# Optimization experiments

Hardware: AMD Instinct MI355X
Metric: run time of the kernel (lower is better)

Reference implementation:

```python
import jax, jax.numpy as jnp
import numpy as np

B, S, HID = 1, 2048, 2048
NH = 16
D_NOPE, D_ROPE, D_V = 128, 64, 128
D_QK = D_NOPE + D_ROPE            # 192
KV_R = 512                        # kv_lora_rank
EPS = 1e-6
SCALING = D_QK ** -0.5
NEG = -1e9


def rms_norm(x, w):
    xf = x.astype(jnp.float32)
    var = jnp.mean(xf * xf, axis=-1, keepdims=True)
    return w * (xf * jax.lax.rsqrt(var + EPS)).astype(x.dtype)


def rotate_half(x):
    x1, x2 = jnp.split(x, 2, axis=-1)
    return jnp.concatenate([-x2, x1], axis=-1)


def deinterleave(x):
    # torch: view(..., d//2, 2).transpose(-1, -2).reshape(..., d)
    # => [x0, x2, x4, ..., x1, x3, x5, ...]
    return jnp.concatenate([x[..., 0::2], x[..., 1::2]], axis=-1)


def setup_inputs() -> dict:
    key = jax.random.key(0)
    ks = jax.random.split(key, 6)
    hidden_states = jax.random.normal(ks[0], (B, S, HID), jnp.float32)
    # rotary cos/sin over qk_rope_head_dim
    inv_freq = 1.0 / (10000.0 ** (np.arange(0, D_ROPE, 2, dtype=np.float32) / D_ROPE))
    freqs = np.outer(np.arange(S, dtype=np.float32), inv_freq)   # [S, D_ROPE/2]
    emb = np.concatenate([freqs, freqs], axis=-1)                # [S, D_ROPE]
    cos = jnp.asarray(np.cos(emb), jnp.float32)[None]            # [1, S, D_ROPE]
    sin = jnp.asarray(np.sin(emb), jnp.float32)[None]
    # additive causal mask [1, 1, S, S]
    causal = np.where(np.tril(np.ones((S, S), dtype=bool)), 0.0, NEG).astype(np.float32)
    attention_mask = jnp.asarray(causal)[None, None]
    sc = lambda k, shp: jax.random.normal(k, shp, jnp.float32) * (shp[-1] ** -0.5)
    q_proj_w = sc(ks[1], (NH * D_QK, HID))
    kv_a_proj_w = sc(ks[2], (KV_R + D_ROPE, HID))
    kv_a_ln_w = jnp.ones((KV_R,), jnp.float32)
    kv_b_proj_w = sc(ks[3], (NH * (D_NOPE + D_V), KV_R))
    o_proj_w = sc(ks[4], (HID, NH * D_V))
    return dict(hidden_states=hidden_states, cos=cos, sin=sin,
                attention_mask=attention_mask, q_proj_w=q_proj_w,
                kv_a_proj_w=kv_a_proj_w, kv_a_ln_w=kv_a_ln_w,
                kv_b_proj_w=kv_b_proj_w, o_proj_w=o_proj_w)


def reference(hidden_states, cos, sin, attention_mask,
              q_proj_w, kv_a_proj_w, kv_a_ln_w, kv_b_proj_w, o_proj_w):
    b, s, _ = hidden_states.shape
    # Q projection -> [b, NH, s, D_QK]
    q = (hidden_states @ q_proj_w.T).reshape(b, s, NH, D_QK).transpose(0, 2, 1, 3)
    q_pass, q_rot = q[..., :D_NOPE], q[..., D_NOPE:]
    # compressed KV + shared rope key
    ckv = hidden_states @ kv_a_proj_w.T                           # [b, s, KV_R + D_ROPE]
    k_pass_c, k_rot = ckv[..., :KV_R], ckv[..., KV_R:]
    kv = (rms_norm(k_pass_c, kv_a_ln_w) @ kv_b_proj_w.T)
    kv = kv.reshape(b, s, NH, D_NOPE + D_V).transpose(0, 2, 1, 3)  # [b, NH, s, .]
    k_pass, value_states = kv[..., :D_NOPE], kv[..., D_NOPE:]
    k_rot = k_rot.reshape(b, 1, s, D_ROPE)
    # interleaved RoPE (rope_interleave=True)
    q_rot = deinterleave(q_rot)
    k_rot = deinterleave(k_rot)
    c = cos[:, None]  # [1, 1, s, D_ROPE]
    sn = sin[:, None]
    q_rot = q_rot * c + rotate_half(q_rot) * sn
    k_rot = k_rot * c + rotate_half(k_rot) * sn
    k_rot = jnp.broadcast_to(k_rot, (b, NH, s, D_ROPE))
    query_states = jnp.concatenate([q_pass, q_rot], axis=-1)      # [b, NH, s, D_QK]
    key_states = jnp.concatenate([k_pass, k_rot], axis=-1)
    # eager attention (num_key_value_groups == 1)
    scores = jnp.einsum('bhqd,bhkd->bhqk', query_states, key_states) * SCALING
    scores = scores + attention_mask[:, :, :, :s]
    attn = jax.nn.softmax(scores.astype(jnp.float32), axis=-1).astype(query_states.dtype)
    attn_out = jnp.einsum('bhqk,bhkd->bhqd', attn, value_states)  # [b, NH, s, D_V]
    attn_out = attn_out.transpose(0, 2, 1, 3).reshape(b, s, NH * D_V)
    return attn_out @ o_proj_w.T
```

## Files before the change

### kernel.cpp

```cpp
#include <hip/hip_runtime.h>
#include <hip/hip_bf16.h>
#include <stdint.h>
#include <stddef.h>

#define S_LEN 2048
#define HID_DIM 2048
#define NH 16
#define D_QK 192
#define D_NOPE 128
#define D_ROPE 64
#define D_V 128
#define KV_R 512
#define CKV_N (KV_R + D_ROPE)
#define KVB_N (NH * (D_NOPE + D_V))
#define QN (NH * D_QK)
#define CAT_N (QN + CKV_N)
#define SCALING 0.07216878364870322f

typedef __attribute__((ext_vector_type(8))) short short8;
typedef __attribute__((ext_vector_type(4))) short short4v;
typedef __attribute__((ext_vector_type(4))) float f32x4;

__device__ __forceinline__ short f2bf_bits(float f) {
  unsigned u = __float_as_uint(f);
  unsigned r = (u + 0x7fffu + ((u >> 16) & 1u)) >> 16;
  return (short)(r & 0xffffu);
}
__device__ __forceinline__ float bf2f(short b) {
  return __uint_as_float(((unsigned)(unsigned short)b) << 16);
}

__device__ __forceinline__ f32x4 mfma_bf16(short8 a, short8 b, f32x4 c) {
  return __builtin_amdgcn_mfma_f32_16x16x32_bf16(a, b, c, 0, 0, 0);
}

__global__ __launch_bounds__(256)
void cvt5_k(const float* __restrict__ s0, short* __restrict__ d0, int c0,
            const float* __restrict__ s1, short* __restrict__ d1, int c1,
            const float* __restrict__ s2, short* __restrict__ d2, int c2,
            const float* __restrict__ s3, short* __restrict__ d3, int c3,
            const float* __restrict__ s4, short* __restrict__ d4, int c4) {
  const int i = blockIdx.x * 256 + threadIdx.x;
  const float* s; short* d; int base;
  if      (i < c0) { s = s0; d = d0; base = 0;  }
  else if (i < c1) { s = s1; d = d1; base = c0; }
  else if (i < c2) { s = s2; d = d2; base = c1; }
  else if (i < c3) { s = s3; d = d3; base = c2; }
  else if (i < c4) { s = s4; d = d4; base = c3; }
  else return;
  const int j = i - base;
  const float4 v = ((const float4*)s)[j];
  short4v o;
  o.x = f2bf_bits(v.x); o.y = f2bf_bits(v.y);
  o.z = f2bf_bits(v.z); o.w = f2bf_bits(v.w);
  ((short4v*)d)[j] = o;
}

template <bool OUTF32>
__global__ __launch_bounds__(256, 3)
void gemm_bt(const short* __restrict__ A, const short* __restrict__ B,
             void* __restrict__ Cv, int M, int N, int K) {
  __shared__ short sA[2][128 * 32];
  __shared__ short sB[2][128 * 32];
  const int tid  = threadIdx.x;
  const int wave = tid >> 6;
  const int lane = tid & 63;
  const int bm = blockIdx.y * 128;
  const int bn = blockIdx.x * 128;
  const int wr = wave >> 1, wc = wave & 1;
  const int fr = lane & 15, fk = (lane >> 4) * 8;
  const int srow = lane >> 2;
  const int scol = (lane & 3) * 8;

  f32x4 acc[4][4];
  for (int i = 0; i < 4; ++i)
    for (int j = 0; j < 4; ++j)
      for (int r = 0; r < 4; ++r) acc[i][j][r] = 0.f;

  for (int k0 = 0; k0 < K; k0 += 64) {
    __syncthreads();
#pragma unroll
    for (int cc = 0; cc < 2; ++cc) {
      const int c = wave * 2 + cc;
      const int ar = bm + c * 16 + srow;
      int br = bn + c * 16 + srow; if (br > N - 1) br = N - 1;
#pragma unroll
      for (int kh = 0; kh < 2; ++kh) {
        __builtin_amdgcn_global_load_lds(
            (const __attribute__((address_space(1))) void*)(A + (size_t)ar * K + k0 + kh * 32 + scol),
            (__attribute__((address_space(3))) void*)(sA[kh] + c * 512), 16, 0, 0);
        __builtin_amdgcn_global_load_lds(
            (const __attribute__((address_space(1))) void*)(B + (size_t)br * K + k0 + kh * 32 + scol),
            (__attribute__((address_space(3))) void*)(sB[kh] + c * 512), 16, 0, 0);
      }
    }
    __syncthreads();
#pragma unroll
    for (int kh = 0; kh < 2; ++kh) {
      short8 af[4], bfr[4];
#pragma unroll
      for (int i = 0; i < 4; ++i)
        af[i] = *(const short8*)(sA[kh] + (wr * 64 + i * 16 + fr) * 32 + fk);
#pragma unroll
      for (int j = 0; j < 4; ++j)
        bfr[j] = *(const short8*)(sB[kh] + (wc * 64 + j * 16 + fr) * 32 + fk);
#pragma unroll
      for (int i = 0; i < 4; ++i)
#pragma unroll
        for (int j = 0; j < 4; ++j)
          acc[i][j] = mfma_bf16(af[i], bfr[j], acc[i][j]);
    }
  }

  const int cr = (lane >> 4) * 4, ccol = lane & 15;
#pragma unroll
  for (int i = 0; i < 4; ++i)
#pragma unroll
    for (int j = 0; j < 4; ++j) {
      const int col = bn + wc * 64 + j * 16 + ccol;
      if (col < N) {
#pragma unroll
        for (int r = 0; r < 4; ++r) {
          const int row = bm + wr * 64 + i * 16 + cr + r;
          if (OUTF32)
            ((float*)Cv)[(size_t)row * N + col] = acc[i][j][r];
          else
            ((short*)Cv)[(size_t)row * N + col] = f2bf_bits(acc[i][j][r]);
        }
      }
    }
}

__global__ __launch_bounds__(256)
void rmsnorm_k(const short* __restrict__ qckv, const float* __restrict__ w,
               short* __restrict__ out) {
  const int s = blockIdx.x, t = threadIdx.x;
  const short* x = qckv + (size_t)s * CAT_N + QN;
  float v0 = bf2f(x[2 * t]), v1 = bf2f(x[2 * t + 1]);
  float ss = v0 * v0 + v1 * v1;
#pragma unroll
  for (int off = 1; off < 64; off <<= 1) ss += __shfl_xor(ss, off, 64);
  __shared__ float red[4];
  if ((t & 63) == 0) red[t >> 6] = ss;
  __syncthreads();
  const float tot = red[0] + red[1] + red[2] + red[3];
  const float sc = rsqrtf(tot * (1.0f / 512.0f) + 1e-6f);
  out[(size_t)s * KV_R + 2 * t]     = f2bf_bits(v0 * sc * w[2 * t]);
  out[(size_t)s * KV_R + 2 * t + 1] = f2bf_bits(v1 * sc * w[2 * t + 1]);
}

__global__ __launch_bounds__(256)
void prep_k(const short* __restrict__ qckv, const short* __restrict__ kvb,
            const float* __restrict__ cosb, const float* __restrict__ sinb,
            short* __restrict__ Qs, short* __restrict__ Ks) {
  const int s = blockIdx.x, t = threadIdx.x;
  const short* qrow = qckv + (size_t)s * CAT_N;
  __shared__ float cs[32], sn[32];
  __shared__ short krs[64];
  if (t < 32) {
    const float c  = cosb[(size_t)s * 64 + t];
    const float si = sinb[(size_t)s * 64 + t];
    cs[t] = c; sn[t] = si;
    const float e0 = bf2f(qrow[QN + KV_R + 2 * t]);
    const float e1 = bf2f(qrow[QN + KV_R + 2 * t + 1]);
    krs[t]      = f2bf_bits(e0 * c - e1 * si);
    krs[t + 32] = f2bf_bits(e1 * c + e0 * si);
  }
  __syncthreads();
  const int h = t >> 4, i = t & 15;
  *(short8*)(Qs + ((size_t)h * S_LEN + s) * D_QK + i * 8) =
      *(const short8*)(qrow + h * D_QK + i * 8);
  *(short8*)(Ks + ((size_t)h * S_LEN + s) * D_QK + i * 8) =
      *(const short8*)(kvb + (size_t)s * KVB_N + h * 256 + i * 8);
#pragma unroll
  for (int p = 0; p < 2; ++p) {
    const int ii = i * 2 + p;
    const float e0 = bf2f(qrow[h * D_QK + 128 + 2 * ii]);
    const float e1 = bf2f(qrow[h * D_QK + 128 + 2 * ii + 1]);
    Qs[((size_t)h * S_LEN + s) * D_QK + 128 + ii] = f2bf_bits(e0 * cs[ii] - e1 * sn[ii]);
    Qs[((size_t)h * S_LEN + s) * D_QK + 160 + ii] = f2bf_bits(e1 * cs[ii] + e0 * sn[ii]);
  }
#pragma unroll
  for (int p = 0; p < 4; ++p) {
    const int idx = t * 4 + p;
    const int hh = idx >> 6, ii = idx & 63;
    Ks[((size_t)hh * S_LEN + s) * D_QK + 128 + ii] = krs[ii];
  }
}

__global__ __launch_bounds__(256)
void vtr_k(const short* __restrict__ kvb, short* __restrict__ Vt) {
  const int st = blockIdx.x, dt = blockIdx.y, h = blockIdx.z;
  __shared__ short sT[64][72];
  const int id = threadIdx.x;
#pragma unroll
  for (int p = 0; p < 2; ++p) {
    const int q = id + p * 256;
    const int row = q >> 3, c8 = q & 7;
    *(short8*)(&sT[row][c8 * 8]) =
        *(const short8*)(kvb + (size_t)(st * 64 + row) * KVB_N + h * 256 + 128 + dt * 64 + c8 * 8);
  }
  __syncthreads();
#pragma unroll
  for (int p = 0; p < 2; ++p) {
    const int q = id + p * 256;
    const int drow = q >> 3, c8 = q & 7;
    short8 o;
#pragma unroll
    for (int j = 0; j < 8; ++j) o[j] = sT[c8 * 8 + j][drow];
    *(short8*)(Vt + ((size_t)h * D_V + dt * 64 + drow) * S_LEN + st * 64 + c8 * 8) = o;
  }
}

__global__ __launch_bounds__(256, 1)
void flash_k(const short* __restrict__ Qs, const short* __restrict__ Ks,
             const short* __restrict__ Vt, short* __restrict__ Oc) {
  __shared__ short sK[64 * 200];
  __shared__ short sVt[128 * 72];
  __shared__ short P_lds[4][16 * 72];
  const int tid = threadIdx.x;
  const int wv = tid >> 6;
  const int lane = tid & 63;
  const int blk = blockIdx.x;
  const int h = ((blk & 7) << 1) | ((blk >> 3) & 1);
  const int a = blk >> 4;
  const int b = 31 - a;
  const int fr = lane & 15, g = lane >> 4;
  const int q0[2] = { a * 64 + wv * 16, b * 64 + wv * 16 };

  const short* Qh = Qs + (size_t)h * S_LEN * D_QK;
  const short* Kh = Ks + (size_t)h * S_LEN * D_QK;
  const short* Vh = Vt + (size_t)h * D_V * S_LEN;

  int rowK[6], c8K[6], rowV[4], c8V[4];
#pragma unroll
  for (int p = 0; p < 6; ++p) {
    const int id = tid + p * 256;
    rowK[p] = id / 24; c8K[p] = id % 24;
  }
#pragma unroll
  for (int p = 0; p < 4; ++p) {
    const int id = tid + p * 256;
    rowV[p] = id >> 3; c8V[p] = id & 7;
  }

  short8 qa[2][6];
#pragma unroll
  for (int rt = 0; rt < 2; ++rt)
#pragma unroll
    for (int c = 0; c < 6; ++c)
      qa[rt][c] = *(const short8*)(Qh + (size_t)(q0[rt] + fr) * D_QK + c * 32 + g * 8);

  f32x4 o[2][8];
  float m_i[2][4], l_i[2][4];
#pragma unroll
  for (int rt = 0; rt < 2; ++rt)
#pragma unroll
    for (int r = 0; r < 4; ++r) {
      m_i[rt][r] = -1e30f; l_i[rt][r] = 0.f;
#pragma unroll
      for (int f = 0; f < 8; ++f) o[rt][f][r] = 0.f;
    }

  short8 kc[6], vc[4];
#pragma unroll
  for (int p = 0; p < 6; ++p)
    kc[p] = *(const short8*)(Kh + (size_t)rowK[p] * D_QK + c8K[p] * 8);
#pragma unroll
  for (int p = 0; p < 4; ++p)
    vc[p] = *(const short8*)(Vh + (size_t)rowV[p] * S_LEN + c8V[p] * 8);

  short* pl = &P_lds[wv][0];
  const int jn = b + 1;
  for (int jt = 0; jt < jn; ++jt) {
    const int j0 = jt << 6;
    const bool lightOn = (jt <= a);
    __syncthreads();
#pragma unroll
    for (int p = 0; p < 6; ++p)
      *(short8*)(sK + rowK[p] * 200 + c8K[p] * 8) = kc[p];
#pragma unroll
    for (int p = 0; p < 4; ++p)
      *(short8*)(sVt + rowV[p] * 72 + c8V[p] * 8) = vc[p];
    __syncthreads();
    if (jt + 1 < jn) {
      const int j1 = (jt + 1) << 6;
#pragma unroll
      for (int p = 0; p < 6; ++p)
        kc[p] = *(const short8*)(Kh + (size_t)(j1 + rowK[p]) * D_QK + c8K[p] * 8);
#pragma unroll
      for (int p = 0; p < 4; ++p)
        vc[p] = *(const short8*)(Vh + (size_t)rowV[p] * S_LEN + j1 + c8V[p] * 8);
    }

    f32x4 sc[2][4];
#pragma unroll
    for (int rt = 0; rt < 2; ++rt)
#pragma unroll
      for (int t = 0; t < 4; ++t)
        for (int r = 0; r < 4; ++r) sc[rt][t][r] = -1e30f;
#pragma unroll
    for (int t = 0; t < 4; ++t) {
      const bool hOn = (j0 + t * 16 <= q0[1] + 15);
      const bool lOn = lightOn && (j0 + t * 16 <= q0[0] + 15);
      if (hOn || lOn) {
        short8 kfr[6];
#pragma unroll
        for (int c = 0; c < 6; ++c)
          kfr[c] = *(const short8*)(sK + (t * 16 + fr) * 200 + c * 32 + g * 8);
        if (lOn) {
          f32x4 acc; for (int r = 0; r < 4; ++r) acc[r] = 0.f;
#pragma unroll
          for (int c = 0; c < 6; ++c) acc = mfma_bf16(qa[0][c], kfr[c], acc);
          sc[0][t] = acc;
        }
        if (hOn) {
          f32x4 acc; for (int r = 0; r < 4; ++r) acc[r] = 0.f;
#pragma unroll
          for (int c = 0; c < 6; ++c) acc = mfma_bf16(qa[1][c], kfr[c], acc);
          sc[1][t] = acc;
        }
      }
    }

#pragma unroll
    for (int rt = 0; rt < 2; ++rt) {
      if (rt == 0 && !lightOn) continue;
      const int qq = q0[rt];
      float tm[4];
#pragma unroll
      for (int r = 0; r < 4; ++r) {
        const int row = qq + g * 4 + r;
        float mx = -1e30f;
#pragma unroll
        for (int t = 0; t < 4; ++t) {
          const float v = (j0 + t * 16 + fr <= row) ? sc[rt][t][r] * SCALING : -1e30f;
          sc[rt][t][r] = v;
          mx = fmaxf(mx, v);
        }
        tm[r] = mx;
      }
#pragma unroll
      for (int off = 1; off < 16; off <<= 1)
#pragma unroll
        for (int r = 0; r < 4; ++r)
          tm[r] = fmaxf(tm[r], __shfl_xor(tm[r], off, 16));
      float ps[4];
#pragma unroll
      for (int r = 0; r < 4; ++r) {
        const float mnew = fmaxf(m_i[rt][r], tm[r]);
        const float alpha = __expf(m_i[rt][r] - mnew);
        m_i[rt][r] = mnew;
        l_i[rt][r] *= alpha;
        float s = 0.f;
#pragma unroll
        for (int t = 0; t < 4; ++t) {
          const float p = __expf(sc[rt][t][r] - mnew);
          sc[rt][t][r] = p;
          s += p;
        }
        ps[r] = s;
#pragma unroll
        for (int f = 0; f < 8; ++f) o[rt][f][r] *= alpha;
      }
#pragma unroll
      for (int off = 1; off < 16; off <<= 1)
#pragma unroll
        for (int r = 0; r < 4; ++r)
          ps[r] += __shfl_xor(ps[r], off, 16);
#pragma unroll
      for (int r = 0; r < 4; ++r) l_i[rt][r] += ps[r];

#pragma unroll
      for (int r = 0; r < 4; ++r)
#pragma unroll
        for (int t = 0; t < 4; ++t)
          pl[(g * 4 + r) * 72 + t * 16 + fr] = f2bf_bits(sc[rt][t][r]);
      __builtin_amdgcn_fence(__ATOMIC_ACQ_REL, "wavefront");
      const short8 pa0 = *(const short8*)(pl + fr * 72 + g * 8);
      const short8 pa1 = *(const short8*)(pl + fr * 72 + 32 + g * 8);
#pragma unroll
      for (int f = 0; f < 8; ++f) {
        const short* vr = sVt + (f * 16 + fr) * 72 + g * 8;
        const short8 vb0 = *(const short8*)(vr);
        const short8 vb1 = *(const short8*)(vr + 32);
        o[rt][f] = mfma_bf16(pa1, vb1, mfma_bf16(pa0, vb0, o[rt][f]));
      }
    }
  }

#pragma unroll
  for (int rt = 0; rt < 2; ++rt)
#pragma unroll
    for (int r = 0; r < 4; ++r) {
      const float inv = 1.0f / l_i[rt][r];
      const int row = q0[rt] + g * 4 + r;
#pragma unroll
      for (int f = 0; f < 8; ++f)
        Oc[(size_t)row * (NH * D_V) + h * D_V + f * 16 + fr] = f2bf_bits(o[rt][f][r] * inv);
    }
}

extern "C" void kernel_launch(void* const* d_in, const int* in_sizes, int n_in,
                              void* d_out, int out_size, void* d_ws, size_t ws_size,
                              hipStream_t stream) {
  const float* hidden = (const float*)d_in[0];
  const float* cosb   = (const float*)d_in[1];
  const float* sinb   = (const float*)d_in[2];
  const float* q_w    = (const float*)d_in[4];
  const float* kva_w  = (const float*)d_in[5];
  const float* ln_w   = (const float*)d_in[6];
  const float* kvb_w  = (const float*)d_in[7];
  const float* o_w    = (const float*)d_in[8];
  float* out = (float*)d_out;

  char* ws = (char*)d_ws;
  size_t off = 0;
  auto alloc = [&](size_t elems) {
    short* p = (short*)(ws + off);
    off += ((elems * 2 + 255) & ~(size_t)255);
    return p;
  };
  short* hid_b   = alloc((size_t)S_LEN * HID_DIM);
  short* qkva_wb = alloc((size_t)CAT_N * HID_DIM);
  short* kvb_wb  = alloc((size_t)KVB_N * KV_R);
  short* o_wb    = alloc((size_t)HID_DIM * NH * D_V);
  short* qckv    = alloc((size_t)S_LEN * CAT_N);
  short* ckvn    = alloc((size_t)S_LEN * KV_R);
  short* kvb     = alloc((size_t)S_LEN * KVB_N);
  short* Qs      = alloc((size_t)NH * S_LEN * D_QK);
  short* Ks      = alloc((size_t)NH * S_LEN * D_QK);
  short* Vt      = alloc((size_t)NH * D_V * S_LEN);
  short* Oc      = alloc((size_t)S_LEN * NH * D_V);

  dim3 blk(256);
  const int n0 = (S_LEN * HID_DIM) / 4;
  const int n1 = (QN * HID_DIM) / 4;
  const int n2 = (CKV_N * HID_DIM) / 4;
  const int n3 = (KVB_N * KV_R) / 4;
  const int n4e = (HID_DIM * NH * D_V) / 4;
  const int c0 = n0, c1 = c0 + n1, c2 = c1 + n2, c3 = c2 + n3, c4 = c3 + n4e;
  cvt5_k<<<dim3((c4 + 255) / 256), blk, 0, stream>>>(
      hidden, hid_b, c0,
      q_w, qkva_wb, c1,
      kva_w, qkva_wb + (size_t)QN * HID_DIM, c2,
      kvb_w, kvb_wb, c3,
      o_w, o_wb, c4);

  gemm_bt<false><<<dim3((CAT_N + 127) / 128, S_LEN / 128), blk, 0, stream>>>(
      hid_b, qkva_wb, qckv, S_LEN, CAT_N, HID_DIM);
  rmsnorm_k<<<dim3(S_LEN), blk, 0, stream>>>(qckv, ln_w, ckvn);
  gemm_bt<false><<<dim3(KVB_N / 128, S_LEN / 128), blk, 0, stream>>>(
      ckvn, kvb_wb, kvb, S_LEN, KVB_N, KV_R);
  prep_k<<<dim3(S_LEN), blk, 0, stream>>>(qckv, kvb, cosb, sinb, Qs, Ks);
  vtr_k<<<dim3(S_LEN / 64, D_V / 64, NH), blk, 0, stream>>>(kvb, Vt);
  flash_k<<<dim3(NH * 16), blk, 0, stream>>>(Qs, Ks, Vt, Oc);
  gemm_bt<true><<<dim3(HID_DIM / 128, S_LEN / 128), blk, 0, stream>>>(
      Oc, o_wb, out, S_LEN, HID_DIM, NH * D_V);
}
```

Baseline: 321.1 us.

## Split paired causal query tiles into one tile per block with higher occupancy

The flash attention kernel previously gave each block two 64-row query tiles (a light one and a heavy one paired for causal load balance). Now each block handles a single query tile, the grid grows from 256 to 512 blocks, and launch bounds allow two blocks per CU. This halves per-thread register state so more waves can hide latency and more CUs get work, at the cost of uneven per-block work and each block reloading K/V tiles on its own with no sharing between the two tiles.

```diff
diff --git a/kernel.cpp b/kernel.cpp
--- a/kernel.cpp
+++ b/kernel.cpp
@@ -212,7 +212,7 @@
   }
 }
 
-__global__ __launch_bounds__(256, 1)
+__global__ __launch_bounds__(256, 2)
 void flash_k(const short* __restrict__ Qs, const short* __restrict__ Ks,
              const short* __restrict__ Vt, short* __restrict__ Oc) {
   __shared__ short sK[64 * 200];
@@ -223,10 +223,9 @@
   const int lane = tid & 63;
   const int blk = blockIdx.x;
   const int h = ((blk & 7) << 1) | ((blk >> 3) & 1);
-  const int a = blk >> 4;
-  const int b = 31 - a;
+  const int qb = 31 - (blk >> 4);
+  const int q0 = qb * 64 + wv * 16;
   const int fr = lane & 15, g = lane >> 4;
-  const int q0[2] = { a * 64 + wv * 16, b * 64 + wv * 16 };
 
   const short* Qh = Qs + (size_t)h * S_LEN * D_QK;
   const short* Kh = Ks + (size_t)h * S_LEN * D_QK;
@@ -244,23 +243,16 @@
     rowV[p] = id >> 3; c8V[p] = id & 7;
   }
 
-  short8 qa[2][6];
-#pragma unroll
-  for (int rt = 0; rt < 2; ++rt)
-#pragma unroll
-    for (int c = 0; c < 6; ++c)
-      qa[rt][c] = *(const short8*)(Qh + (size_t)(q0[rt] + fr) * D_QK + c * 32 + g * 8);
-
-  f32x4 o[2][8];
-  float m_i[2][4], l_i[2][4];
-#pragma unroll
-  for (int rt = 0; rt < 2; ++rt)
-#pragma unroll
-    for (int r = 0; r < 4; ++r) {
-      m_i[rt][r] = -1e30f; l_i[rt][r] = 0.f;
-#pragma unroll
-      for (int f = 0; f < 8; ++f) o[rt][f][r] = 0.f;
-    }
+  short8 qa[6];
+#pragma unroll
+  for (int c = 0; c < 6; ++c)
+    qa[c] = *(const short8*)(Qh + (size_t)(q0 + fr) * D_QK + c * 32 + g * 8);
+
+  f32x4 o[8];
+  for (int f = 0; f < 8; ++f)
+    for (int r = 0; r < 4; ++r) o[f][r] = 0.f;
+  float m_i[4] = {-1e30f, -1e30f, -1e30f, -1e30f};
+  float l_i[4] = {0.f, 0.f, 0.f, 0.f};
 
   short8 kc[6], vc[4];
 #pragma unroll
@@ -271,10 +263,9 @@
     vc[p] = *(const short8*)(Vh + (size_t)rowV[p] * S_LEN + c8V[p] * 8);
 
   short* pl = &P_lds[wv][0];
-  const int jn = b + 1;
+  const int jn = qb + 1;
   for (int jt = 0; jt < jn; ++jt) {
     const int j0 = jt << 6;
-    const bool lightOn = (jt <= a);
     __syncthreads();
 #pragma unroll
     for (int p = 0; p < 6; ++p)
@@ -293,112 +284,92 @@
         vc[p] = *(const short8*)(Vh + (size_t)rowV[p] * S_LEN + j1 + c8V[p] * 8);
     }
 
-    f32x4 sc[2][4];
-#pragma unroll
-    for (int rt = 0; rt < 2; ++rt)
+    f32x4 sc[4];
+#pragma unroll
+    for (int t = 0; t < 4; ++t)
+      for (int r = 0; r < 4; ++r) sc[t][r] = -1e30f;
+#pragma unroll
+    for (int t = 0; t < 4; ++t) {
+      if (j0 + t * 16 <= q0 + 15) {
+        f32x4 a;
+        for (int r = 0; r < 4; ++r) a[r] = 0.f;
+        const short* kr = sK + (t * 16 + fr) * 200 + g * 8;
+#pragma unroll
+        for (int c = 0; c < 6; ++c)
+          a = mfma_bf16(qa[c], *(const short8*)(kr + c * 32), a);
+        sc[t] = a;
+      }
+    }
+    float tm[4];
+#pragma unroll
+    for (int r = 0; r < 4; ++r) {
+      const int row = q0 + g * 4 + r;
+      float mx = -1e30f;
+#pragma unroll
+      for (int t = 0; t < 4; ++t) {
+        const float v = (j0 + t * 16 + fr <= row) ? sc[t][r] * SCALING : -1e30f;
+        sc[t][r] = v;
+        mx = fmaxf(mx, v);
+      }
+      tm[r] = mx;
+    }
+#pragma unroll
+    for (int off = 1; off < 16; off <<= 1)
+#pragma unroll
+      for (int r = 0; r < 4; ++r)
+        tm[r] = fmaxf(tm[r], __shfl_xor(tm[r], off, 16));
+    float ps[4];
+#pragma unroll
+    for (int r = 0; r < 4; ++r) {
+      const float mnew = fmaxf(m_i[r], tm[r]);
+      const float alpha = __expf(m_i[r] - mnew);
+      m_i[r] = mnew;
+      l_i[r] *= alpha;
+      float s = 0.f;
+#pragma unroll
+      for (int t = 0; t < 4; ++t) {
+        const float p = __expf(sc[t][r] - mnew);
+        sc[t][r] = p;
+        s += p;
+      }
+      ps[r] = s;
+#pragma unroll
+      for (int f = 0; f < 8; ++f) o[f][r] *= alpha;
+    }
+#pragma unroll
+    for (int off = 1; off < 16; off <<= 1)
+#pragma unroll
+      for (int r = 0; r < 4; ++r)
+        ps[r] += __shfl_xor(ps[r], off, 16);
+#pragma unroll
+    for (int r = 0; r < 4; ++r) l_i[r] += ps[r];
+
+#pragma unroll
+    for (int r = 0; r < 4; ++r)
 #pragma unroll
       for (int t = 0; t < 4; ++t)
-        for (int r = 0; r < 4; ++r) sc[rt][t][r] = -1e30f;
-#pragma unroll
-    for (int t = 0; t < 4; ++t) {
-      const bool hOn = (j0 + t * 16 <= q0[1] + 15);
-      const bool lOn = lightOn && (j0 + t * 16 <= q0[0] + 15);
-      if (hOn || lOn) {
-        short8 kfr[6];
-#pragma unroll
-        for (int c = 0; c < 6; ++c)
-          kfr[c] = *(const short8*)(sK + (t * 16 + fr) * 200 + c * 32 + g * 8);
-        if (lOn) {
-          f32x4 acc; for (int r = 0; r < 4; ++r) acc[r] = 0.f;
-#pragma unroll
-          for (int c = 0; c < 6; ++c) acc = mfma_bf16(qa[0][c], kfr[c], acc);
-          sc[0][t] = acc;
-        }
-        if (hOn) {
-          f32x4 acc; for (int r = 0; r < 4; ++r) acc[r] = 0.f;
-#pragma unroll
-          for (int c = 0; c < 6; ++c) acc = mfma_bf16(qa[1][c], kfr[c], acc);
-          sc[1][t] = acc;
-        }
-      }
-    }
-
-#pragma unroll
-    for (int rt = 0; rt < 2; ++rt) {
-      if (rt == 0 && !lightOn) continue;
-      const int qq = q0[rt];
-      float tm[4];
-#pragma unroll
-      for (int r = 0; r < 4; ++r) {
-        const int row = qq + g * 4 + r;
-        float mx = -1e30f;
-#pragma unroll
-        for (int t = 0; t < 4; ++t) {
-          const float v = (j0 + t * 16 + fr <= row) ? sc[rt][t][r] * SCALING : -1e30f;
-          sc[rt][t][r] = v;
-          mx = fmaxf(mx, v);
-        }
-        tm[r] = mx;
-      }
-#pragma unroll
-      for (int off = 1; off < 16; off <<= 1)
-#pragma unroll
-        for (int r = 0; r < 4; ++r)
-          tm[r] = fmaxf(tm[r], __shfl_xor(tm[r], off, 16));
-      float ps[4];
-#pragma unroll
-      for (int r = 0; r < 4; ++r) {
-        const float mnew = fmaxf(m_i[rt][r], tm[r]);
-        const float alpha = __expf(m_i[rt][r] - mnew);
-        m_i[rt][r] = mnew;
-        l_i[rt][r] *= alpha;
-        float s = 0.f;
-#pragma unroll
-        for (int t = 0; t < 4; ++t) {
-          const float p = __expf(sc[rt][t][r] - mnew);
-          sc[rt][t][r] = p;
-          s += p;
-        }
-        ps[r] = s;
-#pragma unroll
-        for (int f = 0; f < 8; ++f) o[rt][f][r] *= alpha;
-      }
-#pragma unroll
-      for (int off = 1; off < 16; off <<= 1)
-#pragma unroll
-        for (int r = 0; r < 4; ++r)
-          ps[r] += __shfl_xor(ps[r], off, 16);
-#pragma unroll
-      for (int r = 0; r < 4; ++r) l_i[rt][r] += ps[r];
-
-#pragma unroll
-      for (int r = 0; r < 4; ++r)
-#pragma unroll
-        for (int t = 0; t < 4; ++t)
-          pl[(g * 4 + r) * 72 + t * 16 + fr] = f2bf_bits(sc[rt][t][r]);
-      __builtin_amdgcn_fence(__ATOMIC_ACQ_REL, "wavefront");
-      const short8 pa0 = *(const short8*)(pl + fr * 72 + g * 8);
-      const short8 pa1 = *(const short8*)(pl + fr * 72 + 32 + g * 8);
-#pragma unroll
-      for (int f = 0; f < 8; ++f) {
-        const short* vr = sVt + (f * 16 + fr) * 72 + g * 8;
-        const short8 vb0 = *(const short8*)(vr);
-        const short8 vb1 = *(const short8*)(vr + 32);
-        o[rt][f] = mfma_bf16(pa1, vb1, mfma_bf16(pa0, vb0, o[rt][f]));
-      }
-    }
-  }
-
-#pragma unroll
-  for (int rt = 0; rt < 2; ++rt)
-#pragma unroll
-    for (int r = 0; r < 4; ++r) {
-      const float inv = 1.0f / l_i[rt][r];
-      const int row = q0[rt] + g * 4 + r;
-#pragma unroll
-      for (int f = 0; f < 8; ++f)
-        Oc[(size_t)row * (NH * D_V) + h * D_V + f * 16 + fr] = f2bf_bits(o[rt][f][r] * inv);
-    }
+        pl[(g * 4 + r) * 72 + t * 16 + fr] = f2bf_bits(sc[t][r]);
+    __builtin_amdgcn_fence(__ATOMIC_ACQ_REL, "wavefront");
+    const short8 pa0 = *(const short8*)(pl + fr * 72 + g * 8);
+    const short8 pa1 = *(const short8*)(pl + fr * 72 + 32 + g * 8);
+
+#pragma unroll
+    for (int f = 0; f < 8; ++f) {
+      const short* vr = sVt + (f * 16 + fr) * 72 + g * 8;
+      const short8 vb0 = *(const short8*)(vr);
+      const short8 vb1 = *(const short8*)(vr + 32);
+      o[f] = mfma_bf16(pa1, vb1, mfma_bf16(pa0, vb0, o[f]));
+    }
+  }
+
+#pragma unroll
+  for (int r = 0; r < 4; ++r) {
+    const float inv = 1.0f / l_i[r];
+    const int row = q0 + g * 4 + r;
+#pragma unroll
+    for (int f = 0; f < 8; ++f)
+      Oc[(size_t)row * (NH * D_V) + h * D_V + f * 16 + fr] = f2bf_bits(o[f][r] * inv);
+  }
 }
 
 extern "C" void kernel_launch(void* const* d_in, const int* in_sizes, int n_in,
@@ -454,7 +425,7 @@
       ckvn, kvb_wb, kvb, S_LEN, KVB_N, KV_R);
   prep_k<<<dim3(S_LEN), blk, 0, stream>>>(qckv, kvb, cosb, sinb, Qs, Ks);
   vtr_k<<<dim3(S_LEN / 64, D_V / 64, NH), blk, 0, stream>>>(kvb, Vt);
-  flash_k<<<dim3(NH * 16), blk, 0, stream>>>(Qs, Ks, Vt, Oc);
+  flash_k<<<dim3(NH * 128 / 4), blk, 0, stream>>>(Qs, Ks, Vt, Oc);
   gemm_bt<true><<<dim3(HID_DIM / 128, S_LEN / 128), blk, 0, stream>>>(
       Oc, o_wb, out, S_LEN, HID_DIM, NH * D_V);
 }
```

Measured after the change: 317.7 us. Within noise of the previous version (-1.0%).
